# Performance work log

Hardware: AMD Instinct MI355X
Metric: run time of the kernel (lower is better)

Reference implementation:

```python
import jax, jax.numpy as jnp
import numpy as np

B, N, K = 2, 32768, 16
D_IN, D_OUT = 8, 32
D_HALF = D_OUT // 2
BLOCK = 1024  # query block size for chunked KNN
EPS = 1e-6    # BatchNorm2d eps in the torch module


def _bn(x, g, b):
    # training-mode BatchNorm over all axes except the trailing channel axis
    axes = tuple(range(x.ndim - 1))
    m = jnp.mean(x, axes, keepdims=True)
    v = jnp.var(x, axes, keepdims=True)
    return (x - m) * jax.lax.rsqrt(v + EPS) * g + b


def _knn_idx(coords, k, block=BLOCK):
    # chunked brute-force KNN: never materializes the full (B,N,N) matrix
    b_, n_, _ = coords.shape
    sq = jnp.sum(coords * coords, -1)  # (B,N)
    q = coords.reshape(b_, n_ // block, block, 3).transpose(1, 0, 2, 3)
    q2 = sq.reshape(b_, n_ // block, block).transpose(1, 0, 2)

    def f(args):
        qi, q2i = args  # (B,block,3), (B,block)
        d = q2i[..., None] + sq[:, None, :] - 2.0 * jnp.einsum('bqc,bnc->bqn', qi, coords)
        return jax.lax.top_k(-d, k)[1]  # (B,block,k) nearest indices

    idx = jax.lax.map(f, (q, q2))  # (nb,B,block,k)
    return idx.transpose(1, 0, 2, 3).reshape(b_, n_, k)


def _lse(coords, feats, idx, Wl, bl, g, b):
    # coords (B,N,3), feats (B,N,C), idx (B,N,K) -> (B,N,K,2C)
    neigh = jax.vmap(lambda c, i: c[i])(coords, idx)            # (B,N,K,3)
    center = jnp.broadcast_to(coords[:, :, None, :], neigh.shape)
    ones = jnp.ones(idx.shape + (1,), coords.dtype)             # torch passes idx only -> dist=1
    cat = jnp.concatenate([center, neigh, center - neigh, ones], -1)  # (B,N,K,10)
    h = jax.nn.relu(_bn(cat @ Wl.T + bl, g, b))                 # (B,N,K,C)
    fexp = jnp.broadcast_to(feats[:, :, None, :], h.shape)
    return jnp.concatenate([h, fexp], -1)


def _attpool(x, Ws, Wp, bp, g, b):
    # x (B,N,K,Cin) -> (B,N,Cout); softmax over K (torch dim=-2 after permute)
    s = jax.nn.softmax(x @ Ws.T, axis=2)
    f = jnp.sum(s * x, 2)                                       # (B,N,Cin)
    return jax.nn.relu(_bn(f @ Wp.T + bp, g, b))


def setup_inputs() -> dict:
    key = jax.random.key(0)
    ks = iter(jax.random.split(key, 40))
    p = lambda *s: jax.random.normal(next(ks), s, jnp.float32) * 0.1
    d = {
        'coords': jax.random.normal(next(ks), (B, N, 3), jnp.float32) * 10.0,
        'features': jax.random.normal(next(ks), (B, D_IN, N, 1), jnp.float32),
        'W1': p(D_HALF, D_IN), 'b1': p(D_HALF),
        'Wl1': p(D_HALF, 10), 'bl1': p(D_HALF),
        'gl1': jnp.ones((D_HALF,), jnp.float32), 'bl1b': jnp.zeros((D_HALF,), jnp.float32),
        'Ws1': p(D_OUT, D_OUT),
        'Wp1': p(D_HALF, D_OUT), 'bp1': p(D_HALF),
        'gp1': jnp.ones((D_HALF,), jnp.float32), 'bp1b': jnp.zeros((D_HALF,), jnp.float32),
        'Wl2': p(D_HALF, 10), 'bl2': p(D_HALF),
        'gl2': jnp.ones((D_HALF,), jnp.float32), 'bl2b': jnp.zeros((D_HALF,), jnp.float32),
        'Ws2': p(D_OUT, D_OUT),
        'Wp2': p(D_OUT, D_OUT), 'bp2': p(D_OUT),
        'gp2': jnp.ones((D_OUT,), jnp.float32), 'bp2b': jnp.zeros((D_OUT,), jnp.float32),
        'W2': p(2 * D_OUT, D_OUT), 'b2': p(2 * D_OUT),
        'Wsc': p(2 * D_OUT, D_IN), 'bsc': p(2 * D_OUT),
        'gsc': jnp.ones((2 * D_OUT,), jnp.float32), 'bscb': jnp.zeros((2 * D_OUT,), jnp.float32),
    }
    return d


def reference(coords, features, W1, b1, Wl1, bl1, gl1, bl1b, Ws1, Wp1, bp1, gp1, bp1b,
              Wl2, bl2, gl2, bl2b, Ws2, Wp2, bp2, gp2, bp2b, W2, b2, Wsc, bsc, gsc, bscb):
    feats = features[:, :, :, 0].transpose(0, 2, 1)             # (B,N,d_in) channel-last
    idx = _knn_idx(jax.lax.stop_gradient(coords), K)            # (B,N,K)
    x = jax.nn.leaky_relu(feats @ W1.T + b1, 0.2)               # mlp1 -> (B,N,d_out/2)
    x = _lse(coords, x, idx, Wl1, bl1, gl1, bl1b)               # (B,N,K,d_out)
    x = _attpool(x, Ws1, Wp1, bp1, gp1, bp1b)                   # (B,N,d_out/2)
    x = _lse(coords, x, idx, Wl2, bl2, gl2, bl2b)               # (B,N,K,d_out)
    x = _attpool(x, Ws2, Wp2, bp2, gp2, bp2b)                   # (B,N,d_out)
    out = x @ W2.T + b2                                         # mlp2 -> (B,N,2*d_out)
    sc = _bn(feats @ Wsc.T + bsc, gsc, bscb)                    # shortcut with BN
    out = jax.nn.leaky_relu(out + sc, 0.01)
    return out.transpose(0, 2, 1)[..., None]                    # (B,2*d_out,N,1)
```

## Files before the change

### kernel.cpp

```cpp
#include <hip/hip_runtime.h>
#include <math.h>

#define NPTS  32768
#define NB    2
#define NQ    (NB*NPTS)
#define KK    16
#define EPS   1e-6f
#define G     16
#define G3    (G*G*G)
#define HB    2048
#define SLOP  0.05f
#define TEPS  1e-3f
#define CAPC  512
#define CAP2  1408
#define INVQK (1.f/(float)((size_t)NQ*KK))
#define INVN  (1.f/(float)NQ)

#define S_L1 0
#define S_L2 32
#define S_P1 64
#define S_P2 96
#define S_SC 160

#define WS_X1     (NQ*16)
#define WS_T2     (NQ*32)
#define WS_T4     (NQ*48)
#define WS_STAT   (NQ*80)
#define WS_COEF   (WS_STAT + 512)
#define WS_GCNT   (WS_STAT + 1024)
#define WS_GSTART (WS_GCNT + 2*G3)
#define WS_CELLID (WS_GSTART + 2*G3)
#define WS_SORTID (WS_CELLID + NQ)
#define WS_CSORT  (WS_SORTID + NQ)
#define WS_BBOX   (WS_CSORT + 4*NQ)
#define WS_HIST   (WS_BBOX + 16)
#define WS_EDGE   (WS_HIST + 6*HB)
#define WS_STARTS WS_HIST
#define WS_FAIL   WS_CELLID
#define WS_PART   WS_CSORT
#define WS_PARTA  WS_T2

#define FB_BAD    (1 << 30)

__device__ __forceinline__ float wred64(float v) {
#pragma unroll
  for (int m = 32; m > 0; m >>= 1) v += __shfl_xor(v, m, 64);
  return v;
}

__device__ __forceinline__ unsigned int encf(float f) {
  unsigned int u = __float_as_uint(f);
  return (u & 0x80000000u) ? ~u : (u | 0x80000000u);
}
__device__ __forceinline__ float decf(unsigned int u) {
  return (u & 0x80000000u) ? __uint_as_float(u & 0x7fffffffu) : __uint_as_float(~u);
}

__device__ __forceinline__ int bs16(const float* e, float x) {
  int c = (x >= e[8]) ? 8 : 0;
  c += (x >= e[c+4]) ? 4 : 0;
  c += (x >= e[c+2]) ? 2 : 0;
  c += (x >= e[c+1]) ? 1 : 0;
  return c;
}

__global__ void k_zero_all(float* __restrict__ stats, int* __restrict__ gcnt,
                           int* __restrict__ hist, unsigned int* __restrict__ bbox,
                           int* __restrict__ failcnt) {
  int i = blockIdx.x*256 + threadIdx.x;
  if (i < 2*G3) gcnt[i] = 0;
  if (i < 6*HB) hist[i] = 0;
  if (i < 320)  stats[i] = 0.f;
  if (i < 12)   bbox[i] = ((i % 6) < 3) ? 0xFFFFFFFFu : 0u;
  if (i == 0)   failcnt[0] = 0;
}

__global__ void k_pred(const float* __restrict__ part, int nblk, int nch,
                       float* __restrict__ stats, int soff) {
  __shared__ float red[256];
  int c = blockIdx.x, tid = threadIdx.x;
  float s = 0.f;
  for (int i = tid; i < nblk; i += 256) s += part[(size_t)i*nch + c];
  red[tid] = s;
  __syncthreads();
  for (int off2 = 128; off2 > 0; off2 >>= 1) {
    if (tid < off2) red[tid] += red[tid + off2];
    __syncthreads();
  }
  if (tid == 0) stats[soff + c] = red[0];
}

__global__ void k_pred2(const float* __restrict__ pa, const float* __restrict__ pb,
                        float* __restrict__ stats) {
  __shared__ float red[256];
  int cb = blockIdx.x, tid = threadIdx.x;
  const float* part; int nblk, nch, soff, c;
  if (cb < 128) { part = pa; nblk = 256;  nch = 128; soff = S_SC; c = cb; }
  else          { part = pb; nblk = 4096; nch = 64;  soff = S_L1; c = cb - 128; }
  float s = 0.f;
  for (int i = tid; i < nblk; i += 256) s += part[(size_t)i*nch + c];
  red[tid] = s;
  __syncthreads();
  for (int off2 = 128; off2 > 0; off2 >>= 1) {
    if (tid < off2) red[tid] += red[tid + off2];
    __syncthreads();
  }
  if (tid == 0) stats[soff + c] = red[0];
}

__global__ void k_bbox(const float* __restrict__ coords, unsigned int* __restrict__ bbox) {
  __shared__ unsigned int rmn[3][4], rmx[3][4];
  int tid = threadIdx.x;
  int t = blockIdx.x*256 + tid;
  int b = t >> 15, n = t & (NPTS-1);
  const float* cb = coords + (size_t)b*(NPTS*3);
  unsigned int e[3] = { encf(cb[n*3+0]), encf(cb[n*3+1]), encf(cb[n*3+2]) };
  unsigned int mn[3] = { e[0], e[1], e[2] }, mx[3] = { e[0], e[1], e[2] };
#pragma unroll
  for (int s = 32; s > 0; s >>= 1) {
#pragma unroll
    for (int a = 0; a < 3; ++a) {
      unsigned int o1 = (unsigned int)__shfl_xor((int)mn[a], s, 64);
      unsigned int o2 = (unsigned int)__shfl_xor((int)mx[a], s, 64);
      mn[a] = mn[a] < o1 ? mn[a] : o1;
      mx[a] = mx[a] > o2 ? mx[a] : o2;
    }
  }
  int wave = tid >> 6, lane = tid & 63;
  if (lane == 0) {
#pragma unroll
    for (int a = 0; a < 3; ++a) { rmn[a][wave] = mn[a]; rmx[a][wave] = mx[a]; }
  }
  __syncthreads();
  if (tid < 3) {
    unsigned int a0 = min(min(rmn[tid][0], rmn[tid][1]), min(rmn[tid][2], rmn[tid][3]));
    unsigned int A0 = max(max(rmx[tid][0], rmx[tid][1]), max(rmx[tid][2], rmx[tid][3]));
    atomicMin(&bbox[b*6 + tid], a0);
    atomicMax(&bbox[b*6 + 3 + tid], A0);
  }
}

__global__ void k_hist(const float* __restrict__ coords, const unsigned int* __restrict__ bbox,
                       int* __restrict__ hist) {
  int t = blockIdx.x*256 + threadIdx.x;
  int b = t >> 15, n = t & (NPTS-1);
  const float* cb = coords + (size_t)b*(NPTS*3);
#pragma unroll
  for (int a = 0; a < 3; ++a) {
    float l = decf(bbox[b*6+a]), h = decf(bbox[b*6+3+a]);
    float ex = (h - l)*(1.f + 4e-7f) + 1e-30f;
    float inv = (float)HB/ex;
    int bin = (int)((cb[n*3+a] - l)*inv);
    bin = min(HB-1, max(0, bin));
    atomicAdd(&hist[(b*3+a)*HB + bin], 1);
  }
}

__global__ void k_edges(const int* __restrict__ hist, const unsigned int* __restrict__ bbox,
                        float* __restrict__ edges) {
  __shared__ int part[256];
  int p = blockIdx.x;
  int b = p/3, a = p - b*3;
  int tid = threadIdx.x;
  const int* h = hist + p*HB;
  int v[8]; int s = 0;
#pragma unroll
  for (int i = 0; i < 8; ++i) { v[i] = h[tid*8 + i]; s += v[i]; }
  part[tid] = s;
  __syncthreads();
  for (int off = 1; off < 256; off <<= 1) {
    int x = part[tid];
    int y = (tid >= off) ? part[tid-off] : 0;
    __syncthreads();
    part[tid] = x + y;
    __syncthreads();
  }
  float l = decf(bbox[b*6+a]), hi = decf(bbox[b*6+3+a]);
  float ex = (hi - l)*(1.f + 4e-7f) + 1e-30f;
  float bw = ex*(1.f/(float)HB);
  int c = part[tid] - s;
#pragma unroll
  for (int i = 0; i < 8; ++i) {
    int lo_c = c; c += v[i];
#pragma unroll
    for (int g = 1; g < G; ++g) {
      int tq = g*(NPTS/G);
      if (lo_c < tq && c >= tq) edges[p*(G+1) + g] = l + bw*(float)(tid*8 + i + 1);
    }
  }
  if (tid == 0) { edges[p*(G+1)] = l; edges[p*(G+1) + G] = hi + fabsf(hi)*1e-6f + 1e-20f; }
}

__global__ void k_bin(const float* __restrict__ coords, const float* __restrict__ edges,
                      int* __restrict__ cellid, int* __restrict__ gcnt) {
  __shared__ float se[3][G+1];
  int tid = threadIdx.x;
  int t = blockIdx.x*256 + tid;
  int b = t >> 15, n = t & (NPTS-1);
  if (tid < 3*(G+1)) se[tid/(G+1)][tid%(G+1)] = edges[b*3*(G+1) + tid];
  __syncthreads();
  const float* cb = coords + (size_t)b*(NPTS*3);
  int c0 = bs16(se[0], cb[n*3+0]);
  int c1 = bs16(se[1], cb[n*3+1]);
  int c2 = bs16(se[2], cb[n*3+2]);
  int cid = b*G3 + (c2*G + c1)*G + c0;
  cellid[t] = cid;
  atomicAdd(&gcnt[cid], 1);
}

__global__ void k_alloc(const int* __restrict__ gcnt, int* __restrict__ gstart,
                        int* __restrict__ starts) {
  __shared__ int part[1024];
  int tid = threadIdx.x;
  int v[8]; int s = 0;
#pragma unroll
  for (int i = 0; i < 8; ++i) { v[i] = gcnt[tid*8 + i]; s += v[i]; }
  part[tid] = s;
  __syncthreads();
  for (int off = 1; off < 1024; off <<= 1) {
    int x = part[tid];
    int y = (tid >= off) ? part[tid-off] : 0;
    __syncthreads();
    part[tid] = x + y;
    __syncthreads();
  }
  int base = part[tid] - s;
#pragma unroll
  for (int i = 0; i < 8; ++i) { gstart[tid*8 + i] = base; starts[tid*8 + i] = base; base += v[i]; }
  if (tid == 1023) starts[2*G3] = NQ;
}

__global__ void k_scatter(const float* __restrict__ coords, const int* __restrict__ cellid,
                          int* __restrict__ gstart, float4* __restrict__ csort,
                          int* __restrict__ sortid) {
  int t = blockIdx.x*256 + threadIdx.x;
  int b = t >> 15, n = t & (NPTS-1);
  const float* cb = coords + (size_t)b*(NPTS*3);
  int cid = cellid[t];
  int pos = atomicAdd(&gstart[cid], 1);
  float x = cb[n*3+0], y = cb[n*3+1], z = cb[n*3+2];
  csort[pos] = make_float4(x, y, z, x*x + y*y + z*z);
  sortid[pos] = n;
}

__launch_bounds__(256)
__global__ void k_cellknn(const float4* __restrict__ csort, const int* __restrict__ sortid,
                          const int* __restrict__ starts, const float* __restrict__ edges,
                          int* __restrict__ oidx, int* __restrict__ faillist,
                          int* __restrict__ failcnt) {
  __shared__ float4 big[CAP2];
  __shared__ float  sbdA[4][64];
  __shared__ int    sbiA[4][64];
  __shared__ int    rs[9], rl[9], pre[10];
  __shared__ int    rs2[25], rl2[25], pre2[26];
  __shared__ int    nfl[4];
  __shared__ int    flq[4][16];
  __shared__ float  flT[4][16];
  int tid = threadIdx.x, lane = tid & 63, w = tid >> 6;
  int blk = blockIdx.x;
  int b = blk >> 12;
  int c = blk & (G3-1);
  int cxi = c & 15, cyi = (c >> 4) & 15, czi = c >> 8;
  const int* st = starts + b*G3;
  float* sbd = &sbdA[w][0];
  int*   sbi = &sbiA[w][0];
  if (tid < 4) nfl[tid] = 0;
  if (tid < 9) {
    int dz = tid/3 - 1, dy = tid%3 - 1;
    int z = czi + dz, y = cyi + dy;
    if (z < 0 || z > G-1 || y < 0 || y > G-1) { rs[tid] = 0; rl[tid] = 0; }
    else {
      int xa = max(cxi-1, 0), xb = min(cxi+1, G-1);
      int c0 = (z*G + y)*G + xa;
      int s0 = st[c0], e0 = st[c0 + (xb - xa) + 1];
      rs[tid] = s0; rl[tid] = e0 - s0;
    }
  }
  __syncthreads();
  if (tid == 0) {
    int acc = 0;
#pragma unroll
    for (int i = 0; i < 9; ++i) { pre[i] = acc; acc += rl[i]; }
    pre[9] = acc;
  }
  __syncthreads();
  int total = pre[9];
  int hs = st[c], he = st[c+1];
  int nq = he - hs;
  if (nq == 0) return;
  bool bad = (total > CAPC) || (total < KK);
  if (!bad) {
    for (int i = tid; i < total; i += 256) {
      int row = 0;
#pragma unroll
      for (int rr = 1; rr < 9; ++rr) row += (i >= pre[rr]);
      int gp = rs[row] + (i - pre[row]);
      big[i] = csort[gp];
    }
  }
  __syncthreads();
  int hoff = pre[4] + (hs - rs[4]);
  float blo[3], bhi[3]; bool blok[3], bhik[3];
  int cc3[3] = {cxi, cyi, czi};
#pragma unroll
  for (int a = 0; a < 3; ++a) {
    const float* e = edges + (b*3 + a)*(G+1);
    blok[a] = cc3[a] > 0;     blo[a] = blok[a] ? e[cc3[a]-1] : 0.f;
    bhik[a] = cc3[a] < G-1;   bhi[a] = bhik[a] ? e[cc3[a]+2] : 0.f;
  }
  for (int q0 = 0; q0 < nq; q0 += 4) {
    int qi = q0 + w;
    if (qi >= nq) continue;
    int t = hs + qi;
    if (bad) {
      if (lane == 0) { int pos = atomicAdd(failcnt, 1); faillist[pos] = t | FB_BAD; }
      continue;
    }
    float4 qv = big[hoff + qi];
    float qx = qv.x, qy = qv.y, qz = qv.z, qsq = qv.w;
    float dreg[8];
#pragma unroll
    for (int s = 0; s < 8; ++s) {
      int i = s*64 + lane;
      float d = 1e30f;
      if (i < total) {
        float4 p = big[i];
        d = qsq + p.w - 2.f*(qx*p.x + qy*p.y + qz*p.z);
      }
      dreg[s] = d;
    }
    float mnl = fminf(fminf(fminf(dreg[0],dreg[1]), fminf(dreg[2],dreg[3])),
                      fminf(fminf(dreg[4],dreg[5]), fminf(dreg[6],dreg[7])));
    float v = mnl;
#pragma unroll
    for (int k2 = 2; k2 <= 64; k2 <<= 1) {
#pragma unroll
      for (int j = k2 >> 1; j > 0; j >>= 1) {
        float o = __shfl_xor(v, j, 64);
        bool keepmin = (((lane & j) == 0) == ((lane & k2) == 0));
        v = keepmin ? fminf(v, o) : fmaxf(v, o);
      }
    }
    float Tp = __shfl(v, 15, 64);
    int cnt = 0;
#pragma unroll
    for (int s = 0; s < 8; ++s) {
      bool take = dreg[s] <= Tp;
      unsigned long long bal = __ballot(take);
      int pos = cnt + __popcll(bal & ((1ull << lane) - 1ull));
      if (take && pos < 64) { sbd[pos] = dreg[s]; sbi[pos] = s*64 + lane; }
      cnt += __popcll(bal);
    }
    if (cnt > 64) {
      if (lane == 0) { int pos = atomicAdd(failcnt, 1); faillist[pos] = t | FB_BAD; }
      continue;
    }
    float dv = (lane < cnt) ? sbd[lane] : 1e30f;
    int   iv = (lane < cnt) ? sbi[lane] : 0x7fffffff;
#pragma unroll
    for (int kk = 2; kk <= 64; kk <<= 1) {
#pragma unroll
      for (int j = kk >> 1; j > 0; j >>= 1) {
        float od = __shfl_xor(dv, j, 64);
        int   oi = __shfl_xor(iv, j, 64);
        bool keepmin = (((lane & j) == 0) == ((lane & kk) == 0));
        bool less = (od < dv) || (od == dv && oi < iv);
        bool take2 = keepmin ? less : !less;
        dv = take2 ? od : dv;
        iv = take2 ? oi : iv;
      }
    }
    float d16v = __shfl(dv, 15, 64);
    int resid = iv;
    float m = 1e30f;
    if (blok[0]) m = fminf(m, qx - blo[0]);
    if (bhik[0]) m = fminf(m, bhi[0] - qx);
    if (blok[1]) m = fminf(m, qy - blo[1]);
    if (bhik[1]) m = fminf(m, bhi[1] - qy);
    if (blok[2]) m = fminf(m, qz - blo[2]);
    if (bhik[2]) m = fminf(m, bhi[2] - qz);
    bool ok = (m > 0.f) && (m*m > d16v + SLOP);
    if (ok) {
      int qn = sortid[t];
      size_t row = ((size_t)(b*NPTS + qn))*KK;
      if (lane < KK) {
        int rowi = 0;
#pragma unroll
        for (int rr = 1; rr < 9; ++rr) rowi += (resid >= pre[rr]);
        int gp = rs[rowi] + (resid - pre[rowi]);
        oidx[row + lane] = sortid[gp];
      }
    } else {
      if (lane == 0) {
        int k2 = nfl[w];
        if (k2 < 16) { flq[w][k2] = t; flT[w][k2] = d16v; nfl[w] = k2 + 1; }
        else { int pos = atomicAdd(failcnt, 1); faillist[pos] = t | FB_BAD; }
      }
    }
  }
  __syncthreads();
  if (bad) return;
  if (nfl[0] + nfl[1] + nfl[2] + nfl[3] == 0) return;

  if (tid < 25) {
    int dz = tid/5 - 2, dy = tid%5 - 2;
    int z = czi + dz, y = cyi + dy;
    if (z < 0 || z > G-1 || y < 0 || y > G-1) { rs2[tid] = 0; rl2[tid] = 0; }
    else {
      int xa = max(cxi-2, 0), xb = min(cxi+2, G-1);
      int c0 = (z*G + y)*G + xa;
      int s0 = st[c0], e0 = st[c0 + (xb - xa) + 1];
      rs2[tid] = s0; rl2[tid] = e0 - s0;
    }
  }
  __syncthreads();
  if (tid == 0) {
    int acc = 0;
#pragma unroll
    for (int i = 0; i < 25; ++i) { pre2[i] = acc; acc += rl2[i]; }
    pre2[25] = acc;
  }
  __syncthreads();
  int total2 = pre2[25];
  if (total2 > CAP2) {
    if (lane == 0) {
      for (int k2 = 0; k2 < nfl[w]; ++k2) {
        int pos = atomicAdd(failcnt, 1); faillist[pos] = flq[w][k2] | FB_BAD;
      }
    }
    return;
  }
  for (int i = tid; i < total2; i += 256) {
    int rowi = 0;
#pragma unroll
    for (int rr = 1; rr < 25; ++rr) rowi += (i >= pre2[rr]);
    int gp = rs2[rowi] + (i - pre2[rowi]);
    big[i] = csort[gp];
  }
  __syncthreads();
  float blo2[3], bhi2[3]; bool blok2[3], bhik2[3];
#pragma unroll
  for (int a = 0; a < 3; ++a) {
    const float* e = edges + (b*3 + a)*(G+1);
    blok2[a] = cc3[a] > 1;     blo2[a] = blok2[a] ? e[cc3[a]-2] : 0.f;
    bhik2[a] = cc3[a] < G-2;   bhi2[a] = bhik2[a] ? e[cc3[a]+3] : 0.f;
  }
  for (int k2 = 0; k2 < nfl[w]; ++k2) {
    int t = flq[w][k2];
    float T0 = flT[w][k2] + TEPS;
    float4 qv = csort[t];
    float qx = qv.x, qy = qv.y, qz = qv.z, qsq = qv.w;
    int cnt = 0;
    for (int base2 = 0; base2 < total2; base2 += 64) {
      int i = base2 + lane;
      bool valid = i < total2;
      float d = 1e30f;
      if (valid) {
        float4 p = big[i];
        d = qsq + p.w - 2.f*(qx*p.x + qy*p.y + qz*p.z);
      }
      bool take = valid && (d <= T0);
      unsigned long long bal = __ballot(take);
      int pos = cnt + __popcll(bal & ((1ull << lane) - 1ull));
      if (take && pos < 64) { sbd[pos] = d; sbi[pos] = i; }
      cnt += __popcll(bal);
    }
    if (cnt > 64) {
      if (lane == 0) { int pos = atomicAdd(failcnt, 1); faillist[pos] = t | FB_BAD; }
      continue;
    }
    float dv = (lane < cnt) ? sbd[lane] : 1e30f;
    int   iv = (lane < cnt) ? sbi[lane] : 0x7fffffff;
#pragma unroll
    for (int kk = 2; kk <= 64; kk <<= 1) {
#pragma unroll
      for (int j = kk >> 1; j > 0; j >>= 1) {
        float od = __shfl_xor(dv, j, 64);
        int   oi = __shfl_xor(iv, j, 64);
        bool keepmin = (((lane & j) == 0) == ((lane & kk) == 0));
        bool less = (od < dv) || (od == dv && oi < iv);
        bool take2 = keepmin ? less : !less;
        dv = take2 ? od : dv;
        iv = take2 ? oi : iv;
      }
    }
    float d16b = __shfl(dv, 15, 64);
    float m = 1e30f;
    if (blok2[0]) m = fminf(m, qx - blo2[0]);
    if (bhik2[0]) m = fminf(m, bhi2[0] - qx);
    if (blok2[1]) m = fminf(m, qy - blo2[1]);
    if (bhik2[1]) m = fminf(m, bhi2[1] - qy);
    if (blok2[2]) m = fminf(m, qz - blo2[2]);
    if (bhik2[2]) m = fminf(m, bhi2[2] - qz);
    bool ok = (m > 0.f) && (m*m > d16b + SLOP);
    int qn = sortid[t];
    size_t row = ((size_t)(b*NPTS + qn))*KK;
    if (lane < KK) {
      int rowi = 0;
#pragma unroll
      for (int rr = 1; rr < 25; ++rr) rowi += (iv >= pre2[rr]);
      int gp = rs2[rowi] + (iv - pre2[rowi]);
      oidx[row + lane] = ok ? sortid[gp] : gp;
    }
    if (!ok && lane == 0) { int pos = atomicAdd(failcnt, 1); faillist[pos] = t; }
  }
}

__launch_bounds__(256)
__global__ void k_knn_fb(const float4* __restrict__ csort, const int* __restrict__ sortid,
                         const int* __restrict__ starts, const float* __restrict__ edges,
                         const int* __restrict__ faillist, const int* __restrict__ failcnt,
                         int* __restrict__ oidx) {
  int tid = threadIdx.x, lane = tid & 63, w = tid >> 6;
  int gw = blockIdx.x*4 + w, nw = gridDim.x*4;
  int nf = failcnt[0];
  for (int f = gw; f < nf; f += nw) {
    int fv = faillist[f];
    bool seeded = (fv & FB_BAD) == 0;
    int t = fv & (FB_BAD - 1);
    int b = t >> 15;
    const int* st = starts + b*G3;
    const float* ex = edges + (b*3+0)*(G+1);
    const float* ey = edges + (b*3+1)*(G+1);
    const float* ez = edges + (b*3+2)*(G+1);
    float4 qv = csort[t];
    const float qx = qv.x, qy = qv.y, qz = qv.z, qsq = qv.w;
    int qn = sortid[t];
    size_t row = ((size_t)(b*NPTS + qn))*KK;
    float T;
    int lo_pos, hi_pos;
    if (seeded) {
      float sd = -1e30f;
      if (lane < KK) {
        int pos = oidx[row + lane];
        float4 p = csort[pos];
        sd = qsq + p.w - 2.f*(qx*p.x + qy*p.y + qz*p.z);
      }
      T = sd;
#pragma unroll
      for (int m = 32; m > 0; m >>= 1) T = fmaxf(T, __shfl_xor(T, m, 64));
      T += TEPS;
      float R = sqrtf(T)*1.0001f + 1e-12f;
      bool tk = (lane < G-1) && (ex[lane+1] < qx - R);
      int xl = __popcll(__ballot(tk));
      tk = (lane >= 1 && lane <= G-1) && (ex[lane] > qx + R);
      int xh = (G-1) - __popcll(__ballot(tk));
      tk = (lane < G-1) && (ey[lane+1] < qy - R);
      int yl = __popcll(__ballot(tk));
      tk = (lane >= 1 && lane <= G-1) && (ey[lane] > qy + R);
      int yh = (G-1) - __popcll(__ballot(tk));
      tk = (lane < G-1) && (ez[lane+1] < qz - R);
      int zl = __popcll(__ballot(tk));
      tk = (lane >= 1 && lane <= G-1) && (ez[lane] > qz + R);
      int zh = (G-1) - __popcll(__ballot(tk));
      lo_pos = st[(zl*G + yl)*G + xl];
      hi_pos = st[(zh*G + yh)*G + xh + 1];
    } else {
      float mn = 1e30f;
      for (int i = b*NPTS + lane; i < b*NPTS + NPTS; i += 64) {
        float4 p = csort[i];
        float d = qsq + p.w - 2.f*(qx*p.x + qy*p.y + qz*p.z);
        mn = fminf(mn, d);
      }
      float v = mn;
#pragma unroll
      for (int k2 = 2; k2 <= 64; k2 <<= 1) {
#pragma unroll
        for (int j = k2 >> 1; j > 0; j >>= 1) {
          float o = __shfl_xor(v, j, 64);
          bool keepmin = (((lane & j) == 0) == ((lane & k2) == 0));
          v = keepmin ? fminf(v, o) : fmaxf(v, o);
        }
      }
      T = __shfl(v, 15, 64) + TEPS;
      lo_pos = b*NPTS;
      hi_pos = b*NPTS + NPTS;
    }
    float dl[KK]; int il[KK];
#pragma unroll
    for (int i = 0; i < KK; ++i) { dl[i] = 1e30f; il[i] = 0x7fffffff; }
    for (int i = lo_pos + lane; i < hi_pos; i += 64) {
      float4 p = csort[i];
      float d = qsq + p.w - 2.f*(qx*p.x + qy*p.y + qz*p.z);
      if (d <= T && d < dl[KK-1]) {
        float cd = d; int ci = i;
#pragma unroll
        for (int i2 = 0; i2 < KK; ++i2) {
          bool sw = cd < dl[i2];
          float td = dl[i2]; int ti = il[i2];
          dl[i2] = sw ? cd : td; il[i2] = sw ? ci : ti;
          cd = sw ? td : cd;    ci = sw ? ti : ci;
        }
      }
    }
    int res = 0;
#pragma unroll
    for (int r = 0; r < KK; ++r) {
      float v = dl[0]; int pi = il[0]; int l = lane;
#pragma unroll
      for (int m = 1; m < 64; m <<= 1) {
        float ov = __shfl_xor(v, m, 64);
        int   op = __shfl_xor(pi, m, 64);
        int   ol = __shfl_xor(l, m, 64);
        bool take = (ov < v) || (ov == v && op < pi);
        v = take ? ov : v; pi = take ? op : pi; l = take ? ol : l;
      }
      if (lane == r) res = pi;
      bool win = (lane == l);
#pragma unroll
      for (int i = 0; i < KK-1; ++i) {
        dl[i] = win ? dl[i+1] : dl[i];
        il[i] = win ? il[i+1] : il[i];
      }
      dl[KK-1] = win ? 1e30f : dl[KK-1];
      il[KK-1] = win ? 0x7fffffff : il[KK-1];
    }
    if (lane < KK) oidx[row + lane] = sortid[res];
  }
}

__global__ void k_stats(const float* __restrict__ features,
                        const float* __restrict__ W1, const float* __restrict__ b1,
                        const float* __restrict__ Wsc, const float* __restrict__ bsc,
                        float* __restrict__ x1, float* __restrict__ ppa,
                        const float* __restrict__ coords, const int* __restrict__ idx,
                        const float* __restrict__ Wl1, const float* __restrict__ bl1,
                        const float* __restrict__ Wl2, const float* __restrict__ bl2,
                        float* __restrict__ ppb) {
  int tid = threadIdx.x;
  if (blockIdx.x < 256) {
    __shared__ float sW1[128], sb1[16], sWsc[512], sbsc[64];
    __shared__ float part[128];
    if (tid < 128) { sW1[tid] = W1[tid]; part[tid] = 0.f; }
    if (tid < 16)  sb1[tid] = b1[tid];
    if (tid < 64)  sbsc[tid] = bsc[tid];
    for (int i = tid; i < 512; i += 256) sWsc[i] = Wsc[i];
    __syncthreads();
    int q = blockIdx.x*256 + tid;
    int b = q >> 15, n = q & (NPTS-1);
    float f[8];
#pragma unroll
    for (int c = 0; c < 8; ++c) f[c] = features[((size_t)b*8 + c)*NPTS + n];
#pragma unroll
    for (int co = 0; co < 16; ++co) {
      float a = sb1[co];
#pragma unroll
      for (int c = 0; c < 8; ++c) a += f[c]*sW1[co*8+c];
      x1[(size_t)q*16 + co] = a > 0.f ? a : 0.2f*a;
    }
    int lane = tid & 63;
#pragma unroll
    for (int co = 0; co < 64; ++co) {
      float a = sbsc[co];
#pragma unroll
      for (int c = 0; c < 8; ++c) a += f[c]*sWsc[co*8+c];
      float s = wred64(a), ss = wred64(a*a);
      if (lane == 0) { atomicAdd(&part[co], s); atomicAdd(&part[64+co], ss); }
    }
    __syncthreads();
    if (tid < 128) ppa[(size_t)blockIdx.x*128 + tid] = part[tid];
  } else {
    __shared__ float sW1[160], sb1[16], sW2[160], sb2[16];
    __shared__ float red[4][64];
    int blk = blockIdx.x - 256;
    for (int i = tid; i < 160; i += 256) { sW1[i] = Wl1[i]; sW2[i] = Wl2[i]; }
    if (tid < 16) { sb1[tid] = bl1[tid]; sb2[tid] = bl2[tid]; }
    __syncthreads();
    int t = blk*256 + tid;
    int q = t >> 4;
    int b = q >> 15, n = q & (NPTS-1);
    const float* cb = coords + (size_t)b*(NPTS*3);
    int j = idx[t];
    float cx = cb[n*3], cy = cb[n*3+1], cz = cb[n*3+2];
    float px = cb[j*3], py = cb[j*3+1], pz = cb[j*3+2];
    float cat[10] = {cx,cy,cz,px,py,pz,cx-px,cy-py,cz-pz,1.f};
    int wave = tid >> 6, lane = tid & 63;
#pragma unroll
    for (int co = 0; co < 16; ++co) {
      float a1 = sb1[co], a2 = sb2[co];
#pragma unroll
      for (int d0 = 0; d0 < 10; ++d0) { a1 += cat[d0]*sW1[co*10+d0]; a2 += cat[d0]*sW2[co*10+d0]; }
      float s1 = wred64(a1), q1 = wred64(a1*a1);
      float s2 = wred64(a2), q2 = wred64(a2*a2);
      if (lane == 0) { red[wave][co]=s1; red[wave][16+co]=q1; red[wave][32+co]=s2; red[wave][48+co]=q2; }
    }
    __syncthreads();
    if (tid < 64) {
      float v = red[0][tid] + red[1][tid] + red[2][tid] + red[3][tid];
      ppb[(size_t)blk*64 + tid] = v;
    }
  }
}

__launch_bounds__(256)
__global__ void k_att1(const float* __restrict__ coords, const int* __restrict__ idx,
                       const float* __restrict__ x1ws,
                       const float* __restrict__ Wl1, const float* __restrict__ bl1,
                       const float* __restrict__ Ws1, const float* __restrict__ Wp1,
                       const float* __restrict__ bp1, const float* __restrict__ stats,
                       const float* __restrict__ gl1, const float* __restrict__ bl1b,
                       float* __restrict__ t2, float* __restrict__ ppart) {
  __shared__ float saL[16], scL[16];
  __shared__ float sWl[160], sbl[16];
  __shared__ float sWs[1024];
  __shared__ float sWpT[512], sbp[16];
  __shared__ float lsum[16], lsq[16];
  int tid = threadIdx.x;
  if (tid < 16) {
    float m = stats[S_L1 + tid]*INVQK;
    float v = stats[S_L1 + 16 + tid]*INVQK - m*m;
    float a = gl1[tid]*rsqrtf(v + EPS);
    saL[tid] = a; scL[tid] = bl1b[tid] - m*a;
  }
  __syncthreads();
  for (int i = tid; i < 160; i += 256) { int c = i/10; sWl[i] = Wl1[i]*saL[c]; }
  if (tid < 16) sbl[tid] = bl1[tid]*saL[tid] + scL[tid];
  for (int i = tid; i < 1024; i += 256) sWs[i] = Ws1[i];
  for (int i = tid; i < 512; i += 256) { int co = i >> 4, cp = i & 15; sWpT[i] = Wp1[cp*32 + co]; }
  if (tid < 16) { sbp[tid] = bp1[tid]; lsum[tid] = 0.f; lsq[tid] = 0.f; }
  __syncthreads();
  int gp = blockIdx.x*16 + (tid >> 4);
  int k  = tid & 15;
  int b = gp >> 15, n = gp & (NPTS-1);
  const float* cb = coords + (size_t)b*(NPTS*3);
  int j = idx[(size_t)gp*KK + k];
  float cx = cb[n*3], cy = cb[n*3+1], cz = cb[n*3+2];
  float px = cb[j*3], py = cb[j*3+1], pz = cb[j*3+2];
  float cat[10] = {cx,cy,cz,px,py,pz,cx-px,cy-py,cz-pz,1.f};
  float x[32];
#pragma unroll
  for (int co = 0; co < 16; ++co) {
    float a = sbl[co];
#pragma unroll
    for (int d0 = 0; d0 < 10; ++d0) a += cat[d0]*sWl[co*10+d0];
    x[co] = a > 0.f ? a : 0.f;
  }
  {
    const float4* xp = (const float4*)(x1ws + (size_t)gp*16);
    float4 u0 = xp[0], u1 = xp[1], u2 = xp[2], u3 = xp[3];
    x[16]=u0.x; x[17]=u0.y; x[18]=u0.z; x[19]=u0.w;
    x[20]=u1.x; x[21]=u1.y; x[22]=u1.z; x[23]=u1.w;
    x[24]=u2.x; x[25]=u2.y; x[26]=u2.z; x[27]=u2.w;
    x[28]=u3.x; x[29]=u3.y; x[30]=u3.z; x[31]=u3.w;
  }
  float tacc = sbp[k];
#pragma unroll
  for (int co = 0; co < 32; ++co) {
    float s = 0.f;
#pragma unroll
    for (int ci = 0; ci < 32; ++ci) s += x[ci]*sWs[co*32+ci];
    float m = s;
#pragma unroll
    for (int msk = 8; msk > 0; msk >>= 1) m = fmaxf(m, __shfl_xor(m, msk, 16));
    float e = __expf(s - m);
    float se = e;
#pragma unroll
    for (int msk = 8; msk > 0; msk >>= 1) se += __shfl_xor(se, msk, 16);
    float w = e/se;
    float fv = w*x[co];
#pragma unroll
    for (int msk = 8; msk > 0; msk >>= 1) fv += __shfl_xor(fv, msk, 16);
    tacc += fv*sWpT[co*16+k];
  }
  t2[(size_t)gp*16 + k] = tacc;
  atomicAdd(&lsum[k], tacc);
  atomicAdd(&lsq[k], tacc*tacc);
  __syncthreads();
  if (tid < 16) {
    ppart[(size_t)blockIdx.x*32 + tid]      = lsum[tid];
    ppart[(size_t)blockIdx.x*32 + 16 + tid] = lsq[tid];
  }
}

__launch_bounds__(256)
__global__ void k_att2(const float* __restrict__ coords, const int* __restrict__ idx,
                       const float* __restrict__ t2ws,
                       const float* __restrict__ Wl2, const float* __restrict__ bl2,
                       const float* __restrict__ Ws2, const float* __restrict__ Wp2,
                       const float* __restrict__ bp2, const float* __restrict__ stats,
                       const float* __restrict__ gl2, const float* __restrict__ bl2b,
                       const float* __restrict__ gp1, const float* __restrict__ bp1b,
                       float* __restrict__ t4, float* __restrict__ ppart) {
  __shared__ float saL[16], scL[16];
  __shared__ float sWl[160], sbl[16];
  __shared__ float sWs[1024];
  __shared__ float sWpT[1024], sbp[32];
  __shared__ float sa1[16], sc1[16];
  __shared__ float lsum[32], lsq[32];
  int tid = threadIdx.x;
  if (tid < 16) {
    float m = stats[S_L2 + tid]*INVQK;
    float v = stats[S_L2 + 16 + tid]*INVQK - m*m;
    float a = gl2[tid]*rsqrtf(v + EPS);
    saL[tid] = a; scL[tid] = bl2b[tid] - m*a;
    float m1 = stats[S_P1 + tid]*INVN;
    float v1 = stats[S_P1 + 16 + tid]*INVN - m1*m1;
    float a1 = gp1[tid]*rsqrtf(v1 + EPS);
    sa1[tid] = a1; sc1[tid] = bp1b[tid] - m1*a1;
  }
  __syncthreads();
  for (int i = tid; i < 160; i += 256) { int c = i/10; sWl[i] = Wl2[i]*saL[c]; }
  if (tid < 16) sbl[tid] = bl2[tid]*saL[tid] + scL[tid];
  for (int i = tid; i < 1024; i += 256) {
    sWs[i] = Ws2[i];
    int co = i >> 5, cp = i & 31; sWpT[i] = Wp2[cp*32 + co];
  }
  if (tid < 32) { sbp[tid] = bp2[tid]; lsum[tid]=0.f; lsq[tid]=0.f; }
  __syncthreads();
  int gp = blockIdx.x*16 + (tid >> 4);
  int k  = tid & 15;
  int b = gp >> 15, n = gp & (NPTS-1);
  const float* cb = coords + (size_t)b*(NPTS*3);
  int j = idx[(size_t)gp*KK + k];
  float cx = cb[n*3], cy = cb[n*3+1], cz = cb[n*3+2];
  float px = cb[j*3], py = cb[j*3+1], pz = cb[j*3+2];
  float cat[10] = {cx,cy,cz,px,py,pz,cx-px,cy-py,cz-pz,1.f};
  float x[32];
#pragma unroll
  for (int co = 0; co < 16; ++co) {
    float a = sbl[co];
#pragma unroll
    for (int d0 = 0; d0 < 10; ++d0) a += cat[d0]*sWl[co*10+d0];
    x[co] = a > 0.f ? a : 0.f;
  }
  {
    const float4* xp = (const float4*)(t2ws + (size_t)gp*16);
    float4 u0 = xp[0], u1 = xp[1], u2 = xp[2], u3 = xp[3];
    float xv[16] = {u0.x,u0.y,u0.z,u0.w, u1.x,u1.y,u1.z,u1.w,
                    u2.x,u2.y,u2.z,u2.w, u3.x,u3.y,u3.z,u3.w};
#pragma unroll
    for (int c = 0; c < 16; ++c) {
      float v = xv[c]*sa1[c] + sc1[c];
      x[16+c] = v > 0.f ? v : 0.f;
    }
  }
  float tacc0 = sbp[k], tacc1 = sbp[k+16];
#pragma unroll
  for (int co = 0; co < 32; ++co) {
    float s = 0.f;
#pragma unroll
    for (int ci = 0; ci < 32; ++ci) s += x[ci]*sWs[co*32+ci];
    float m = s;
#pragma unroll
    for (int msk = 8; msk > 0; msk >>= 1) m = fmaxf(m, __shfl_xor(m, msk, 16));
    float e = __expf(s - m);
    float se = e;
#pragma unroll
    for (int msk = 8; msk > 0; msk >>= 1) se += __shfl_xor(se, msk, 16);
    float w = e/se;
    float fv = w*x[co];
#pragma unroll
    for (int msk = 8; msk > 0; msk >>= 1) fv += __shfl_xor(fv, msk, 16);
    tacc0 += fv*sWpT[co*32+k];
    tacc1 += fv*sWpT[co*32+k+16];
  }
  t4[(size_t)gp*32 + k]      = tacc0;
  t4[(size_t)gp*32 + k + 16] = tacc1;
  atomicAdd(&lsum[k], tacc0);      atomicAdd(&lsq[k], tacc0*tacc0);
  atomicAdd(&lsum[k+16], tacc1);   atomicAdd(&lsq[k+16], tacc1*tacc1);
  __syncthreads();
  if (tid < 32) {
    ppart[(size_t)blockIdx.x*64 + tid]      = lsum[tid];
    ppart[(size_t)blockIdx.x*64 + 32 + tid] = lsq[tid];
  }
}

__global__ void k_final(const float* __restrict__ t4ws, const float* __restrict__ features,
                        const float* __restrict__ W2, const float* __restrict__ b2,
                        const float* __restrict__ Wsc, const float* __restrict__ bsc,
                        const float* __restrict__ stats,
                        const float* __restrict__ gsc, const float* __restrict__ bscb,
                        const float* __restrict__ gp2, const float* __restrict__ bp2b,
                        float* __restrict__ out) {
  __shared__ float saS[64], scS[64];
  __shared__ float sW2[2048], sb2[64], sWscF[512], sbscF[64], sa[32], scc[32];
  int tid = threadIdx.x;
  if (tid < 64) {
    float m = stats[S_SC + tid]*INVN;
    float v = stats[S_SC + 64 + tid]*INVN - m*m;
    float a = gsc[tid]*rsqrtf(v + EPS);
    saS[tid] = a; scS[tid] = bscb[tid] - m*a;
  }
  if (tid < 32) {
    float m = stats[S_P2 + tid]*INVN;
    float v = stats[S_P2 + 32 + tid]*INVN - m*m;
    float a = gp2[tid]*rsqrtf(v + EPS);
    sa[tid] = a; scc[tid] = bp2b[tid] - m*a;
  }
  __syncthreads();
  for (int i = tid; i < 2048; i += 256) sW2[i] = W2[i];
  if (tid < 64) sb2[tid] = b2[tid];
  for (int i = tid; i < 512; i += 256) { int c2 = i >> 3; sWscF[i] = Wsc[i]*saS[c2]; }
  if (tid < 64) sbscF[tid] = bsc[tid]*saS[tid] + scS[tid];
  __syncthreads();
  int q = blockIdx.x*256 + tid;
  int b = q >> 15, n = q & (NPTS-1);
  float x3[32];
  const float4* tp = (const float4*)(t4ws + (size_t)q*32);
#pragma unroll
  for (int i = 0; i < 8; ++i) {
    float4 u = tp[i];
    float v0 = u.x*sa[4*i+0] + scc[4*i+0];
    float v1 = u.y*sa[4*i+1] + scc[4*i+1];
    float v2 = u.z*sa[4*i+2] + scc[4*i+2];
    float v3 = u.w*sa[4*i+3] + scc[4*i+3];
    x3[4*i+0] = v0 > 0.f ? v0 : 0.f;
    x3[4*i+1] = v1 > 0.f ? v1 : 0.f;
    x3[4*i+2] = v2 > 0.f ? v2 : 0.f;
    x3[4*i+3] = v3 > 0.f ? v3 : 0.f;
  }
  float f[8];
#pragma unroll
  for (int c = 0; c < 8; ++c) f[c] = features[((size_t)b*8+c)*NPTS + n];
  for (int c2 = 0; c2 < 64; ++c2) {
    float acc = sb2[c2];
#pragma unroll
    for (int co = 0; co < 32; ++co) acc += x3[co]*sW2[c2*32+co];
    float sv = sbscF[c2];
#pragma unroll
    for (int c = 0; c < 8; ++c) sv += f[c]*sWscF[c2*8+c];
    float o = acc + sv;
    out[((size_t)b*64 + c2)*NPTS + n] = o > 0.f ? o : 0.01f*o;
  }
}

extern "C" void kernel_launch(void* const* d_in, const int* in_sizes, int n_in,
                              void* d_out, int out_size, void* d_ws, size_t ws_size,
                              hipStream_t stream) {
  const float* coords   = (const float*)d_in[0];
  const float* features = (const float*)d_in[1];
  const float* W1  = (const float*)d_in[2];
  const float* b1  = (const float*)d_in[3];
  const float* Wl1 = (const float*)d_in[4];
  const float* bl1 = (const float*)d_in[5];
  const float* gl1 = (const float*)d_in[6];
  const float* bl1b= (const float*)d_in[7];
  const float* Ws1 = (const float*)d_in[8];
  const float* Wp1 = (const float*)d_in[9];
  const float* bp1 = (const float*)d_in[10];
  const float* gp1 = (const float*)d_in[11];
  const float* bp1b= (const float*)d_in[12];
  const float* Wl2 = (const float*)d_in[13];
  const float* bl2 = (const float*)d_in[14];
  const float* gl2 = (const float*)d_in[15];
  const float* bl2b= (const float*)d_in[16];
  const float* Ws2 = (const float*)d_in[17];
  const float* Wp2 = (const float*)d_in[18];
  const float* bp2 = (const float*)d_in[19];
  const float* gp2 = (const float*)d_in[20];
  const float* bp2b= (const float*)d_in[21];
  const float* W2  = (const float*)d_in[22];
  const float* b2  = (const float*)d_in[23];
  const float* Wsc = (const float*)d_in[24];
  const float* bsc = (const float*)d_in[25];
  const float* gsc = (const float*)d_in[26];
  const float* bscb= (const float*)d_in[27];

  float* wsF  = (float*)d_ws;
  int*   wsI  = (int*)d_ws;
  int*   idxp = wsI;
  float* x1p  = wsF + WS_X1;
  float* t2p  = wsF + WS_T2;
  float* t4p  = wsF + WS_T4;
  float* stat = wsF + WS_STAT;
  int*   gcnt = wsI + WS_GCNT;
  int*   gsta = wsI + WS_GSTART;
  int*   gcel = wsI + WS_CELLID;
  int*   sid  = wsI + WS_SORTID;
  float4* csrt = (float4*)(wsF + WS_CSORT);
  unsigned int* bbox = (unsigned int*)(wsI + WS_BBOX);
  int*   fcnt = wsI + WS_BBOX + 12;
  int*   flist= wsI + WS_FAIL;
  int*   hist = wsI + WS_HIST;
  int*   strt = wsI + WS_STARTS;
  float* edge = wsF + WS_EDGE;
  float* prt  = wsF + WS_PART;
  float* prtA = wsF + WS_PARTA;
  float* outp = (float*)d_out;

  hipLaunchKernelGGL(k_zero_all, dim3(48), dim3(256), 0, stream, stat, gcnt, hist, bbox, fcnt);
  hipLaunchKernelGGL(k_bbox,    dim3(NQ/256), dim3(256), 0, stream, coords, bbox);
  hipLaunchKernelGGL(k_hist,    dim3(NQ/256), dim3(256), 0, stream, coords, bbox, hist);
  hipLaunchKernelGGL(k_edges,   dim3(6), dim3(256), 0, stream, hist, bbox, edge);
  hipLaunchKernelGGL(k_bin,     dim3(NQ/256), dim3(256), 0, stream, coords, edge, gcel, gcnt);
  hipLaunchKernelGGL(k_alloc,   dim3(1), dim3(1024), 0, stream, gcnt, gsta, strt);
  hipLaunchKernelGGL(k_scatter, dim3(NQ/256), dim3(256), 0, stream, coords, gcel, gsta, csrt, sid);
  hipLaunchKernelGGL(k_cellknn, dim3(2*G3), dim3(256), 0, stream,
                     csrt, sid, strt, edge, idxp, flist, fcnt);
  hipLaunchKernelGGL(k_knn_fb,  dim3(2048), dim3(256), 0, stream,
                     csrt, sid, strt, edge, flist, fcnt, idxp);
  hipLaunchKernelGGL(k_stats, dim3(256 + (NQ*KK)/256), dim3(256), 0, stream,
                     features, W1, b1, Wsc, bsc, x1p, prtA,
                     coords, idxp, Wl1, bl1, Wl2, bl2, prt);
  hipLaunchKernelGGL(k_pred2, dim3(192), dim3(256), 0, stream, prtA, prt, stat);
  hipLaunchKernelGGL(k_att1, dim3(NQ/16), dim3(256), 0, stream,
                     coords, idxp, x1p, Wl1, bl1, Ws1, Wp1, bp1, stat, gl1, bl1b, t2p, prt);
  hipLaunchKernelGGL(k_pred, dim3(32), dim3(256), 0, stream, prt, NQ/16, 32, stat, S_P1);
  hipLaunchKernelGGL(k_att2, dim3(NQ/16), dim3(256), 0, stream,
                     coords, idxp, t2p, Wl2, bl2, Ws2, Wp2, bp2, stat,
                     gl2, bl2b, gp1, bp1b, t4p, prt);
  hipLaunchKernelGGL(k_pred, dim3(64), dim3(256), 0, stream, prt, NQ/16, 64, stat, S_P2);
  hipLaunchKernelGGL(k_final, dim3(NQ/256), dim3(256), 0, stream,
                     t4p, features, W2, b2, Wsc, bsc, stat, gsc, bscb, gp2, bp2b, outp);
}
```

Before: 805.8 us.

## Process two KNN queries per wavefront using 32-lane half-waves

The cell KNN kernel now splits each 64-lane wavefront into two 32-lane halves, each handling its own query. Each lane evaluates 16 candidate distances instead of 8, and the threshold and top-K bitonic sorts run over 32 lanes within each half. This halves the number of query-loop iterations and shortens the shuffle sort networks. In exchange, the candidate buffer per query is capped at 32 instead of 64 while the threshold comes from fewer lane minima, so more queries may overflow and fall back to the slower failure path.

```diff
diff --git a/kernel.cpp b/kernel.cpp
--- a/kernel.cpp
+++ b/kernel.cpp
@@ -257,6 +257,7 @@
   __shared__ int    flq[4][16];
   __shared__ float  flT[4][16];
   int tid = threadIdx.x, lane = tid & 63, w = tid >> 6;
+  int l5 = lane & 31, h = lane >> 5;
   int blk = blockIdx.x;
   int b = blk >> 12;
   int c = blk & (G3-1);
@@ -308,70 +309,75 @@
     blok[a] = cc3[a] > 0;     blo[a] = blok[a] ? e[cc3[a]-1] : 0.f;
     bhik[a] = cc3[a] < G-1;   bhi[a] = bhik[a] ? e[cc3[a]+2] : 0.f;
   }
-  for (int q0 = 0; q0 < nq; q0 += 4) {
-    int qi = q0 + w;
-    if (qi >= nq) continue;
-    int t = hs + qi;
+  unsigned long long hmask = h ? 0xFFFFFFFF00000000ull : 0x00000000FFFFFFFFull;
+  for (int q0 = 0; q0 < nq; q0 += 8) {
+    int qi = q0 + 2*w + h;
+    bool act = qi < nq;
+    int tq = hs + qi;
     if (bad) {
-      if (lane == 0) { int pos = atomicAdd(failcnt, 1); faillist[pos] = t | FB_BAD; }
+      if (lane == 0) {
+        int qA = q0 + 2*w, qB = qA + 1;
+        if (qA < nq) { int pos = atomicAdd(failcnt, 1); faillist[pos] = (hs+qA) | FB_BAD; }
+        if (qB < nq) { int pos = atomicAdd(failcnt, 1); faillist[pos] = (hs+qB) | FB_BAD; }
+      }
       continue;
     }
-    float4 qv = big[hoff + qi];
+    if (q0 + 2*w >= nq) continue;
+    float4 qv = big[hoff + (act ? qi : 0)];
     float qx = qv.x, qy = qv.y, qz = qv.z, qsq = qv.w;
-    float dreg[8];
-#pragma unroll
-    for (int s = 0; s < 8; ++s) {
-      int i = s*64 + lane;
+    float dreg[16];
+#pragma unroll
+    for (int s = 0; s < 16; ++s) {
+      int i = s*32 + l5;
       float d = 1e30f;
-      if (i < total) {
+      if (act && i < total) {
         float4 p = big[i];
         d = qsq + p.w - 2.f*(qx*p.x + qy*p.y + qz*p.z);
       }
       dreg[s] = d;
     }
-    float mnl = fminf(fminf(fminf(dreg[0],dreg[1]), fminf(dreg[2],dreg[3])),
-                      fminf(fminf(dreg[4],dreg[5]), fminf(dreg[6],dreg[7])));
+    float m0 = fminf(fminf(dreg[0],dreg[1]),   fminf(dreg[2],dreg[3]));
+    float m1 = fminf(fminf(dreg[4],dreg[5]),   fminf(dreg[6],dreg[7]));
+    float m2 = fminf(fminf(dreg[8],dreg[9]),   fminf(dreg[10],dreg[11]));
+    float m3 = fminf(fminf(dreg[12],dreg[13]), fminf(dreg[14],dreg[15]));
+    float mnl = fminf(fminf(m0,m1), fminf(m2,m3));
     float v = mnl;
 #pragma unroll
-    for (int k2 = 2; k2 <= 64; k2 <<= 1) {
+    for (int k2 = 2; k2 <= 32; k2 <<= 1) {
 #pragma unroll
       for (int j = k2 >> 1; j > 0; j >>= 1) {
         float o = __shfl_xor(v, j, 64);
-        bool keepmin = (((lane & j) == 0) == ((lane & k2) == 0));
+        bool keepmin = (((l5 & j) == 0) == ((l5 & k2) == 0));
         v = keepmin ? fminf(v, o) : fmaxf(v, o);
       }
     }
-    float Tp = __shfl(v, 15, 64);
+    float Tp = __shfl(v, (lane & 32) + 15, 64);
     int cnt = 0;
 #pragma unroll
-    for (int s = 0; s < 8; ++s) {
-      bool take = dreg[s] <= Tp;
+    for (int s = 0; s < 16; ++s) {
+      bool take = act && (dreg[s] <= Tp);
       unsigned long long bal = __ballot(take);
-      int pos = cnt + __popcll(bal & ((1ull << lane) - 1ull));
-      if (take && pos < 64) { sbd[pos] = dreg[s]; sbi[pos] = s*64 + lane; }
-      cnt += __popcll(bal);
-    }
-    if (cnt > 64) {
-      if (lane == 0) { int pos = atomicAdd(failcnt, 1); faillist[pos] = t | FB_BAD; }
-      continue;
-    }
-    float dv = (lane < cnt) ? sbd[lane] : 1e30f;
-    int   iv = (lane < cnt) ? sbi[lane] : 0x7fffffff;
-#pragma unroll
-    for (int kk = 2; kk <= 64; kk <<= 1) {
+      int pos = cnt + __popcll(bal & hmask & ((1ull << lane) - 1ull));
+      if (take && pos < 32) { sbd[pos + 32*h] = dreg[s]; sbi[pos + 32*h] = s*32 + l5; }
+      cnt += __popcll(bal & hmask);
+    }
+    bool over = act && (cnt > 32);
+    float dv = (l5 < cnt) ? sbd[l5 + 32*h] : 1e30f;
+    int   iv = (l5 < cnt) ? sbi[l5 + 32*h] : 0x7fffffff;
+#pragma unroll
+    for (int kk = 2; kk <= 32; kk <<= 1) {
 #pragma unroll
       for (int j = kk >> 1; j > 0; j >>= 1) {
         float od = __shfl_xor(dv, j, 64);
         int   oi = __shfl_xor(iv, j, 64);
-        bool keepmin = (((lane & j) == 0) == ((lane & kk) == 0));
+        bool keepmin = (((l5 & j) == 0) == ((l5 & kk) == 0));
         bool less = (od < dv) || (od == dv && oi < iv);
         bool take2 = keepmin ? less : !less;
         dv = take2 ? od : dv;
         iv = take2 ? oi : iv;
       }
     }
-    float d16v = __shfl(dv, 15, 64);
-    int resid = iv;
+    float d16v = __shfl(dv, (lane & 32) + 15, 64);
     float m = 1e30f;
     if (blok[0]) m = fminf(m, qx - blo[0]);
     if (bhik[0]) m = fminf(m, bhi[0] - qx);
@@ -379,22 +385,32 @@
     if (bhik[1]) m = fminf(m, bhi[1] - qy);
     if (blok[2]) m = fminf(m, qz - blo[2]);
     if (bhik[2]) m = fminf(m, bhi[2] - qz);
-    bool ok = (m > 0.f) && (m*m > d16v + SLOP);
-    if (ok) {
-      int qn = sortid[t];
+    bool ok = act && !over && (m > 0.f) && (m*m > d16v + SLOP);
+    if (ok && l5 < KK) {
+      int qn = sortid[tq];
       size_t row = ((size_t)(b*NPTS + qn))*KK;
-      if (lane < KK) {
-        int rowi = 0;
-#pragma unroll
-        for (int rr = 1; rr < 9; ++rr) rowi += (resid >= pre[rr]);
-        int gp = rs[rowi] + (resid - pre[rowi]);
-        oidx[row + lane] = sortid[gp];
-      }
-    } else {
-      if (lane == 0) {
+      int rowi = 0;
+#pragma unroll
+      for (int rr = 1; rr < 9; ++rr) rowi += (iv >= pre[rr]);
+      int gp = rs[rowi] + (iv - pre[rowi]);
+      oidx[row + l5] = sortid[gp];
+    }
+    bool pushbad = act && over;
+    bool pushfl  = act && !over && !ok;
+    if (lane == 0) {
+      if (pushbad) { int pos = atomicAdd(failcnt, 1); faillist[pos] = tq | FB_BAD; }
+      else if (pushfl) {
         int k2 = nfl[w];
-        if (k2 < 16) { flq[w][k2] = t; flT[w][k2] = d16v; nfl[w] = k2 + 1; }
-        else { int pos = atomicAdd(failcnt, 1); faillist[pos] = t | FB_BAD; }
+        if (k2 < 16) { flq[w][k2] = tq; flT[w][k2] = d16v; nfl[w] = k2 + 1; }
+        else { int pos = atomicAdd(failcnt, 1); faillist[pos] = tq | FB_BAD; }
+      }
+    }
+    if (lane == 32) {
+      if (pushbad) { int pos = atomicAdd(failcnt, 1); faillist[pos] = tq | FB_BAD; }
+      else if (pushfl) {
+        int k2 = nfl[w];
+        if (k2 < 16) { flq[w][k2] = tq; flT[w][k2] = d16v; nfl[w] = k2 + 1; }
+        else { int pos = atomicAdd(failcnt, 1); faillist[pos] = tq | FB_BAD; }
       }
     }
   }
```

New measurement: 826.6 us. 1.03x slower.
